# Kernel optimization log

Hardware: AMD Instinct MI355X
Metric: run time of the kernel (lower is better)

The kernel has to match this reference:

```python
import jax, jax.numpy as jnp
import numpy as np

NUM_NODES = 4000
SEQ_LEN = 96
LATENT_DIM = 32
GCN_LAYERS = 2
B = 4
NT = NUM_NODES + SEQ_LEN  # 4096


def setup_inputs() -> dict:
    key = jax.random.key(0)
    k_x, k_w = jax.random.split(key)
    X = jax.random.normal(k_x, (B, NT, LATENT_DIM), dtype=jnp.float32) * 0.1
    # per-layer weights for the graph conv (HeteroFASTGCN-style message passing)
    W = jax.random.normal(k_w, (GCN_LAYERS, LATENT_DIM, LATENT_DIM), dtype=jnp.float32) * (1.0 / np.sqrt(LATENT_DIM))
    return {"X": X, "W": W}


def reference(X, W):
    # STGraphConstructor: node_embs = concat(spatial, temporal) == X
    # adj = tanh(relu(X X^T) + I); dense equivalent of the per-batch nonzero
    # edge extraction (sparse edges carry exactly the nonzero adj entries,
    # so weighted scatter-aggregation == adj @ H).
    sim = jnp.einsum('bnf,bmf->bnm', X, X)          # (B, NT, NT)
    eye = jnp.eye(NT, dtype=X.dtype)
    adj = jnp.tanh(jax.nn.relu(sim) + eye)
    # graph conv: gcn_layers of weighted aggregation + linear + elu
    H = X
    for l in range(GCN_LAYERS):
        H = jax.nn.elu(jnp.einsum('bnm,bmf,fg->bng', adj, H, W[l]))
    # GraphEmbeeding is identity on H
    return H
```

## Files before the change

kernel.cpp:

```cpp
#include <hip/hip_runtime.h>

#define NTOT 4096
#define FD 32
#define BATCH 4

typedef __attribute__((ext_vector_type(8))) _Float16 half8;
typedef __attribute__((ext_vector_type(4))) _Float16 half4;
typedef __attribute__((ext_vector_type(2))) _Float16 half2v;
typedef __attribute__((ext_vector_type(4))) float f32x4;

__device__ __forceinline__ float tanh_pos(float t) {
    float u = __builtin_amdgcn_exp2f(t * 2.885390081777927f);
    float r = __builtin_amdgcn_rcpf(u + 1.0f);
    return __builtin_fmaf(-2.0f, r, 1.0f);
}

__device__ __forceinline__ float tanh_poly_f32(float t) {
    float t2 = t * t;
    float c = __builtin_fmaf(t2, 0.1333333333f, -0.3333333333f);
    return __builtin_fmaf(t * t2, c, t);
}

__device__ __forceinline__ float eluf(float x) {
    return x > 0.0f ? x : (__builtin_amdgcn_exp2f(x * 1.4426950408889634f) - 1.0f);
}

__device__ __forceinline__ half4 pack_relu_poly(f32x4 s) {
    half2v a = __builtin_bit_cast(half2v, __builtin_amdgcn_cvt_pkrtz(s[0], s[1]));
    half2v b = __builtin_bit_cast(half2v, __builtin_amdgcn_cvt_pkrtz(s[2], s[3]));
    const half2v zero = {(_Float16)0.0f, (_Float16)0.0f};
    const half2v mth = {(_Float16)(-0.33333334f), (_Float16)(-0.33333334f)};
    const half2v one = {(_Float16)1.0f, (_Float16)1.0f};
    a = __builtin_elementwise_max(a, zero);
    b = __builtin_elementwise_max(b, zero);
    half2v a2 = a * a, b2 = b * b;
    half2v ca = a2 * mth + one, cb = b2 * mth + one;
    a = a * ca;
    b = b * cb;
    return __builtin_shufflevector(a, b, 0, 1, 2, 3);
}

__global__ __launch_bounds__(256) void convert_x(const float* __restrict__ X,
                                                 _Float16* __restrict__ Kfrag,
                                                 _Float16* __restrict__ Vfrag) {
    __shared__ float lds[128 * 33];
    const int tid = threadIdx.x;
    const int blk = blockIdx.x;
    const int xcd = blk & 7;
    const int batch = xcd >> 1;
    const int chunk = ((xcd & 1) << 4) | (blk >> 3);
    const int nbase = chunk << 7;

    const float* Xp = X + ((size_t)batch * NTOT + nbase) * FD;
#pragma unroll
    for (int k = 0; k < 16; ++k) {
        int e = tid + k * 256;
        lds[(e >> 5) * 33 + (e & 31)] = Xp[e];
    }
    __syncthreads();

    {
        _Float16* kout = Kfrag + (size_t)batch * NTOT * FD + (size_t)(nbase >> 4) * 512;
        const int tl = tid >> 5;
        const int l0 = (tid & 31) * 2;
#pragma unroll
        for (int s = 0; s < 2; ++s) {
            int l = l0 + s;
            int row = tl * 16 + (l & 15);
            int cb = (l >> 4) * 8;
            half8 v;
#pragma unroll
            for (int j = 0; j < 8; ++j) v[j] = (_Float16)lds[row * 33 + cb + j];
            *(half8*)(kout + (tl * 64 + l) * 8) = v;
        }
    }
    {
        _Float16* vout = Vfrag + (size_t)batch * NTOT * FD + (size_t)(nbase >> 4) * 512;
        const int tl = tid >> 5;
        const int fh = (tid >> 4) & 1;
        const int lb = (tid & 15) * 4;
#pragma unroll
        for (int li = 0; li < 4; ++li) {
            int lane = lb + li;
            int l15 = lane & 15, lg = lane >> 4;
            half4 v;
#pragma unroll
            for (int j = 0; j < 4; ++j)
                v[j] = (_Float16)lds[(tl * 16 + lg * 4 + j) * 33 + fh * 16 + l15];
            *(half4*)(vout + ((tl * 2 + fh) * 64 + lane) * 4) = v;
        }
    }
}

template <int LAYER>
__global__ __launch_bounds__(512, 4) void gcn_layer_kernel(const _Float16* __restrict__ Kf,
                                                           const _Float16* __restrict__ Vf,
                                                           const float* __restrict__ Wg,
                                                           _Float16* __restrict__ outHt,
                                                           float* __restrict__ outF) {
    __shared__ float lds_part[8 * 32 * 32];

    const int tid = threadIdx.x;
    const int lane = tid & 63;
    const int wv = tid >> 6;
    const int blk = blockIdx.x;
    const int xcd = blk & 7;
    const int b = xcd >> 1;
    const int rowbase = ((((xcd & 1) << 6) + (blk >> 3))) << 5;
    const int l15 = lane & 15;
    const int lg = lane >> 4;

    const _Float16* KfB = Kf + (size_t)b * NTOT * FD;
    const _Float16* VfB = Vf + (size_t)b * NTOT * FD;

    const half8 q1 = *(const half8*)(KfB + (size_t)(rowbase >> 4) * 512 + lane * 8);
    const half8 q2 = *(const half8*)(KfB + (size_t)((rowbase >> 4) + 1) * 512 + lane * 8);

    const int col0 = wv << 9;
    const _Float16* kq = KfB + (size_t)(col0 >> 4) * 512 + lane * 8;
    const _Float16* vq = VfB + (size_t)(col0 >> 4) * 512 + lane * 4;

    f32x4 accA0 = {0.f, 0.f, 0.f, 0.f}, accA1 = {0.f, 0.f, 0.f, 0.f};
    f32x4 accB0 = {0.f, 0.f, 0.f, 0.f}, accB1 = {0.f, 0.f, 0.f, 0.f};
    const f32x4 zero = {0.f, 0.f, 0.f, 0.f};

    const int diag_it = (rowbase - col0) >> 5;

#pragma unroll
    for (int it = 0; it < 16; ++it) {
        half8 k0 = *(const half8*)(kq + it * 1024);
        half8 k1 = *(const half8*)(kq + it * 1024 + 512);
        half4 v00 = *(const half4*)(vq + it * 1024);
        half4 v01 = *(const half4*)(vq + it * 1024 + 256);
        half4 v10 = *(const half4*)(vq + it * 1024 + 512);
        half4 v11 = *(const half4*)(vq + it * 1024 + 768);

        f32x4 s00 = __builtin_amdgcn_mfma_f32_16x16x32_f16(k0, q1, zero, 0, 0, 0);
        f32x4 s01 = __builtin_amdgcn_mfma_f32_16x16x32_f16(k0, q2, zero, 0, 0, 0);
        f32x4 s10 = __builtin_amdgcn_mfma_f32_16x16x32_f16(k1, q1, zero, 0, 0, 0);
        f32x4 s11 = __builtin_amdgcn_mfma_f32_16x16x32_f16(k1, q2, zero, 0, 0, 0);

        half4 p00, p01, p10, p11;
        if (it == diag_it) {
            float t00[4], t01[4], t10[4], t11[4];
#pragma unroll
            for (int e = 0; e < 4; ++e) {
                t00[e] = fmaxf(s00[e], 0.0f);
                t01[e] = fmaxf(s01[e], 0.0f);
                t10[e] = fmaxf(s10[e], 0.0f);
                t11[e] = fmaxf(s11[e], 0.0f);
            }
#pragma unroll
            for (int e = 0; e < 4; ++e) {
                bool d = (lg * 4 + e == l15);
                t00[e] = d ? tanh_pos(t00[e] + 1.0f) : tanh_poly_f32(t00[e]);
                t11[e] = d ? tanh_pos(t11[e] + 1.0f) : tanh_poly_f32(t11[e]);
                t01[e] = tanh_poly_f32(t01[e]);
                t10[e] = tanh_poly_f32(t10[e]);
            }
            p00 = __builtin_shufflevector(
                __builtin_bit_cast(half2v, __builtin_amdgcn_cvt_pkrtz(t00[0], t00[1])),
                __builtin_bit_cast(half2v, __builtin_amdgcn_cvt_pkrtz(t00[2], t00[3])), 0, 1, 2, 3);
            p01 = __builtin_shufflevector(
                __builtin_bit_cast(half2v, __builtin_amdgcn_cvt_pkrtz(t01[0], t01[1])),
                __builtin_bit_cast(half2v, __builtin_amdgcn_cvt_pkrtz(t01[2], t01[3])), 0, 1, 2, 3);
            p10 = __builtin_shufflevector(
                __builtin_bit_cast(half2v, __builtin_amdgcn_cvt_pkrtz(t10[0], t10[1])),
                __builtin_bit_cast(half2v, __builtin_amdgcn_cvt_pkrtz(t10[2], t10[3])), 0, 1, 2, 3);
            p11 = __builtin_shufflevector(
                __builtin_bit_cast(half2v, __builtin_amdgcn_cvt_pkrtz(t11[0], t11[1])),
                __builtin_bit_cast(half2v, __builtin_amdgcn_cvt_pkrtz(t11[2], t11[3])), 0, 1, 2, 3);
        } else {
            p00 = pack_relu_poly(s00);
            p01 = pack_relu_poly(s01);
            p10 = pack_relu_poly(s10);
            p11 = pack_relu_poly(s11);
        }

        accA0 = __builtin_amdgcn_mfma_f32_16x16x16f16(v00, p00, accA0, 0, 0, 0);
        accA1 = __builtin_amdgcn_mfma_f32_16x16x16f16(v00, p01, accA1, 0, 0, 0);
        accB0 = __builtin_amdgcn_mfma_f32_16x16x16f16(v01, p00, accB0, 0, 0, 0);
        accB1 = __builtin_amdgcn_mfma_f32_16x16x16f16(v01, p01, accB1, 0, 0, 0);
        accA0 = __builtin_amdgcn_mfma_f32_16x16x16f16(v10, p10, accA0, 0, 0, 0);
        accA1 = __builtin_amdgcn_mfma_f32_16x16x16f16(v10, p11, accA1, 0, 0, 0);
        accB0 = __builtin_amdgcn_mfma_f32_16x16x16f16(v11, p10, accB0, 0, 0, 0);
        accB1 = __builtin_amdgcn_mfma_f32_16x16x16f16(v11, p11, accB1, 0, 0, 0);
    }

#pragma unroll
    for (int e = 0; e < 4; ++e) {
        int f0 = lg * 4 + e;
        lds_part[(wv * 32 + f0) * 32 + l15] = accA0[e];
        lds_part[(wv * 32 + f0) * 32 + 16 + l15] = accA1[e];
        lds_part[(wv * 32 + 16 + f0) * 32 + l15] = accB0[e];
        lds_part[(wv * 32 + 16 + f0) * 32 + 16 + l15] = accB1[e];
    }
    __syncthreads();

#pragma unroll
    for (int k = 0; k < 2; ++k) {
        int o = tid + k * 512;
        float ssum = 0.0f;
#pragma unroll
        for (int ww = 0; ww < 8; ++ww) ssum += lds_part[ww * 1024 + o];
        lds_part[o] = ssum;
    }
    __syncthreads();

    if (LAYER == 0) {
        const int jp = tid & 1;
        const int vlane = (tid >> 1) & 63;
        const int fh = (tid >> 7) & 1;
        const int tl = tid >> 8;
        const int vl15 = vlane & 15, vlg = vlane >> 4;
        const int g = fh * 16 + vl15;
        const int r0 = tl * 16 + vlg * 4 + jp * 2;
        float a0 = 0.0f, a1 = 0.0f;
#pragma unroll
        for (int f = 0; f < FD; ++f) {
            float w = Wg[f * FD + g];
            a0 = __builtin_fmaf(lds_part[f * 32 + r0], w, a0);
            a1 = __builtin_fmaf(lds_part[f * 32 + r0 + 1], w, a1);
        }
        a0 = eluf(a0);
        a1 = eluf(a1);
        unsigned pk = __builtin_bit_cast(unsigned, __builtin_amdgcn_cvt_pkrtz(a0, a1));
        _Float16* dst = outHt + (size_t)b * NTOT * FD +
                        ((size_t)(((rowbase >> 4) + tl) * 2 + fh) * 64 + vlane) * 4 + jp * 2;
        *(unsigned*)dst = pk;
    } else {
        const int g = tid & 31, r0 = tid >> 5;
        float a0 = 0.0f, a1 = 0.0f;
#pragma unroll
        for (int f = 0; f < FD; ++f) {
            float w = Wg[f * FD + g];
            a0 = __builtin_fmaf(lds_part[f * 32 + r0], w, a0);
            a1 = __builtin_fmaf(lds_part[f * 32 + r0 + 16], w, a1);
        }
        a0 = eluf(a0);
        a1 = eluf(a1);
        float* dst = outF + ((size_t)b * NTOT + rowbase) * FD + g;
        dst[(size_t)r0 * FD] = a0;
        dst[(size_t)(r0 + 16) * FD] = a1;
    }
}

extern "C" void kernel_launch(void* const* d_in, const int* in_sizes, int n_in,
                              void* d_out, int out_size, void* d_ws, size_t ws_size,
                              hipStream_t stream) {
    const float* X = (const float*)d_in[0];
    const float* W = (const float*)d_in[1];
    float* out = (float*)d_out;

    _Float16* Kfrag = (_Float16*)d_ws;
    _Float16* VfragX = Kfrag + (size_t)BATCH * NTOT * FD;
    _Float16* H1frag = VfragX + (size_t)BATCH * NTOT * FD;

    convert_x<<<128, 256, 0, stream>>>(X, Kfrag, VfragX);
    gcn_layer_kernel<0><<<512, 512, 0, stream>>>(Kfrag, VfragX, W, H1frag, nullptr);
    gcn_layer_kernel<1><<<512, 512, 0, stream>>>(Kfrag, H1frag, W + FD * FD, nullptr, out);
}
```

Before: 41.67 us.

## Process 64 rows per block with 16 waves and fp16 partial reduction

Each block now covers 64 query rows using 1024 threads (16 waves), and each wave handles 256 key columns across four query tiles. Every K/V fragment load now feeds four query tiles instead of two, which cuts global traffic per output and halves the grid to 256 blocks. Cross-wave partial sums are stored in LDS as fp16 to fit the larger reduction, at some precision cost. Fewer blocks on a large chip and more registers per thread may reduce occupancy.

```diff
diff --git a/kernel.cpp b/kernel.cpp
--- a/kernel.cpp
+++ b/kernel.cpp
@@ -40,6 +40,20 @@
     return __builtin_shufflevector(a, b, 0, 1, 2, 3);
 }
 
+__device__ __forceinline__ half4 diag_transform(f32x4 s, int l15, int lg) {
+    float t[4];
+#pragma unroll
+    for (int e = 0; e < 4; ++e) t[e] = fmaxf(s[e], 0.0f);
+#pragma unroll
+    for (int e = 0; e < 4; ++e) {
+        bool d = (lg * 4 + e == l15);
+        t[e] = d ? tanh_pos(t[e] + 1.0f) : tanh_poly_f32(t[e]);
+    }
+    return __builtin_shufflevector(
+        __builtin_bit_cast(half2v, __builtin_amdgcn_cvt_pkrtz(t[0], t[1])),
+        __builtin_bit_cast(half2v, __builtin_amdgcn_cvt_pkrtz(t[2], t[3])), 0, 1, 2, 3);
+}
+
 __global__ __launch_bounds__(256) void convert_x(const float* __restrict__ X,
                                                  _Float16* __restrict__ Kfrag,
                                                  _Float16* __restrict__ Vfrag) {
@@ -93,12 +107,12 @@
 }
 
 template <int LAYER>
-__global__ __launch_bounds__(512, 4) void gcn_layer_kernel(const _Float16* __restrict__ Kf,
-                                                           const _Float16* __restrict__ Vf,
-                                                           const float* __restrict__ Wg,
-                                                           _Float16* __restrict__ outHt,
-                                                           float* __restrict__ outF) {
-    __shared__ float lds_part[8 * 32 * 32];
+__global__ __launch_bounds__(1024, 4) void gcn_layer_kernel(const _Float16* __restrict__ Kf,
+                                                            const _Float16* __restrict__ Vf,
+                                                            const float* __restrict__ Wg,
+                                                            _Float16* __restrict__ outHt,
+                                                            float* __restrict__ outF) {
+    __shared__ _Float16 lds_part[16 * 64 * 32];
 
     const int tid = threadIdx.x;
     const int lane = tid & 63;
@@ -106,127 +120,119 @@
     const int blk = blockIdx.x;
     const int xcd = blk & 7;
     const int b = xcd >> 1;
-    const int rowbase = ((((xcd & 1) << 6) + (blk >> 3))) << 5;
+    const int rowidx = ((xcd & 1) << 5) | (blk >> 3);
+    const int rowbase = rowidx << 6;
     const int l15 = lane & 15;
     const int lg = lane >> 4;
 
     const _Float16* KfB = Kf + (size_t)b * NTOT * FD;
     const _Float16* VfB = Vf + (size_t)b * NTOT * FD;
 
-    const half8 q1 = *(const half8*)(KfB + (size_t)(rowbase >> 4) * 512 + lane * 8);
-    const half8 q2 = *(const half8*)(KfB + (size_t)((rowbase >> 4) + 1) * 512 + lane * 8);
-
-    const int col0 = wv << 9;
+    half8 q[4];
+#pragma unroll
+    for (int qt = 0; qt < 4; ++qt)
+        q[qt] = *(const half8*)(KfB + (size_t)((rowbase >> 4) + qt) * 512 + lane * 8);
+
+    const int col0 = wv << 8;
     const _Float16* kq = KfB + (size_t)(col0 >> 4) * 512 + lane * 8;
     const _Float16* vq = VfB + (size_t)(col0 >> 4) * 512 + lane * 4;
 
-    f32x4 accA0 = {0.f, 0.f, 0.f, 0.f}, accA1 = {0.f, 0.f, 0.f, 0.f};
-    f32x4 accB0 = {0.f, 0.f, 0.f, 0.f}, accB1 = {0.f, 0.f, 0.f, 0.f};
+    f32x4 accA[4], accB[4];
+#pragma unroll
+    for (int qt = 0; qt < 4; ++qt) {
+        accA[qt] = (f32x4){0.f, 0.f, 0.f, 0.f};
+        accB[qt] = (f32x4){0.f, 0.f, 0.f, 0.f};
+    }
     const f32x4 zero = {0.f, 0.f, 0.f, 0.f};
 
-    const int diag_it = (rowbase - col0) >> 5;
-
-#pragma unroll
-    for (int it = 0; it < 16; ++it) {
-        half8 k0 = *(const half8*)(kq + it * 1024);
-        half8 k1 = *(const half8*)(kq + it * 1024 + 512);
-        half4 v00 = *(const half4*)(vq + it * 1024);
-        half4 v01 = *(const half4*)(vq + it * 1024 + 256);
-        half4 v10 = *(const half4*)(vq + it * 1024 + 512);
-        half4 v11 = *(const half4*)(vq + it * 1024 + 768);
-
-        f32x4 s00 = __builtin_amdgcn_mfma_f32_16x16x32_f16(k0, q1, zero, 0, 0, 0);
-        f32x4 s01 = __builtin_amdgcn_mfma_f32_16x16x32_f16(k0, q2, zero, 0, 0, 0);
-        f32x4 s10 = __builtin_amdgcn_mfma_f32_16x16x32_f16(k1, q1, zero, 0, 0, 0);
-        f32x4 s11 = __builtin_amdgcn_mfma_f32_16x16x32_f16(k1, q2, zero, 0, 0, 0);
-
-        half4 p00, p01, p10, p11;
-        if (it == diag_it) {
-            float t00[4], t01[4], t10[4], t11[4];
-#pragma unroll
-            for (int e = 0; e < 4; ++e) {
-                t00[e] = fmaxf(s00[e], 0.0f);
-                t01[e] = fmaxf(s01[e], 0.0f);
-                t10[e] = fmaxf(s10[e], 0.0f);
-                t11[e] = fmaxf(s11[e], 0.0f);
-            }
-#pragma unroll
-            for (int e = 0; e < 4; ++e) {
-                bool d = (lg * 4 + e == l15);
-                t00[e] = d ? tanh_pos(t00[e] + 1.0f) : tanh_poly_f32(t00[e]);
-                t11[e] = d ? tanh_pos(t11[e] + 1.0f) : tanh_poly_f32(t11[e]);
-                t01[e] = tanh_poly_f32(t01[e]);
-                t10[e] = tanh_poly_f32(t10[e]);
-            }
-            p00 = __builtin_shufflevector(
-                __builtin_bit_cast(half2v, __builtin_amdgcn_cvt_pkrtz(t00[0], t00[1])),
-                __builtin_bit_cast(half2v, __builtin_amdgcn_cvt_pkrtz(t00[2], t00[3])), 0, 1, 2, 3);
-            p01 = __builtin_shufflevector(
-                __builtin_bit_cast(half2v, __builtin_amdgcn_cvt_pkrtz(t01[0], t01[1])),
-                __builtin_bit_cast(half2v, __builtin_amdgcn_cvt_pkrtz(t01[2], t01[3])), 0, 1, 2, 3);
-            p10 = __builtin_shufflevector(
-                __builtin_bit_cast(half2v, __builtin_amdgcn_cvt_pkrtz(t10[0], t10[1])),
-                __builtin_bit_cast(half2v, __builtin_amdgcn_cvt_pkrtz(t10[2], t10[3])), 0, 1, 2, 3);
-            p11 = __builtin_shufflevector(
-                __builtin_bit_cast(half2v, __builtin_amdgcn_cvt_pkrtz(t11[0], t11[1])),
-                __builtin_bit_cast(half2v, __builtin_amdgcn_cvt_pkrtz(t11[2], t11[3])), 0, 1, 2, 3);
-        } else {
-            p00 = pack_relu_poly(s00);
-            p01 = pack_relu_poly(s01);
-            p10 = pack_relu_poly(s10);
-            p11 = pack_relu_poly(s11);
-        }
-
-        accA0 = __builtin_amdgcn_mfma_f32_16x16x16f16(v00, p00, accA0, 0, 0, 0);
-        accA1 = __builtin_amdgcn_mfma_f32_16x16x16f16(v00, p01, accA1, 0, 0, 0);
-        accB0 = __builtin_amdgcn_mfma_f32_16x16x16f16(v01, p00, accB0, 0, 0, 0);
-        accB1 = __builtin_amdgcn_mfma_f32_16x16x16f16(v01, p01, accB1, 0, 0, 0);
-        accA0 = __builtin_amdgcn_mfma_f32_16x16x16f16(v10, p10, accA0, 0, 0, 0);
-        accA1 = __builtin_amdgcn_mfma_f32_16x16x16f16(v10, p11, accA1, 0, 0, 0);
-        accB0 = __builtin_amdgcn_mfma_f32_16x16x16f16(v11, p10, accB0, 0, 0, 0);
-        accB1 = __builtin_amdgcn_mfma_f32_16x16x16f16(v11, p11, accB1, 0, 0, 0);
-    }
-
-#pragma unroll
-    for (int e = 0; e < 4; ++e) {
-        int f0 = lg * 4 + e;
-        lds_part[(wv * 32 + f0) * 32 + l15] = accA0[e];
-        lds_part[(wv * 32 + f0) * 32 + 16 + l15] = accA1[e];
-        lds_part[(wv * 32 + 16 + f0) * 32 + l15] = accB0[e];
-        lds_part[(wv * 32 + 16 + f0) * 32 + 16 + l15] = accB1[e];
-    }
-    __syncthreads();
-
-#pragma unroll
-    for (int k = 0; k < 2; ++k) {
-        int o = tid + k * 512;
-        float ssum = 0.0f;
-#pragma unroll
-        for (int ww = 0; ww < 8; ++ww) ssum += lds_part[ww * 1024 + o];
-        lds_part[o] = ssum;
-    }
+    const int diagA = (rowbase - col0) >> 5;
+
+#pragma unroll
+    for (int it = 0; it < 8; ++it) {
+        const int base = it * 1024;
+        half8 k0 = *(const half8*)(kq + base);
+        half8 k1 = *(const half8*)(kq + base + 512);
+        half4 v00 = *(const half4*)(vq + base);
+        half4 v01 = *(const half4*)(vq + base + 256);
+        half4 v10 = *(const half4*)(vq + base + 512);
+        half4 v11 = *(const half4*)(vq + base + 768);
+
+        f32x4 s0[4], s1[4];
+#pragma unroll
+        for (int qt = 0; qt < 4; ++qt) {
+            s0[qt] = __builtin_amdgcn_mfma_f32_16x16x32_f16(k0, q[qt], zero, 0, 0, 0);
+            s1[qt] = __builtin_amdgcn_mfma_f32_16x16x32_f16(k1, q[qt], zero, 0, 0, 0);
+        }
+
+        half4 p0[4], p1[4];
+#pragma unroll
+        for (int qt = 0; qt < 4; ++qt) {
+            p0[qt] = pack_relu_poly(s0[qt]);
+            p1[qt] = pack_relu_poly(s1[qt]);
+        }
+        if (it == diagA) {
+            p0[0] = diag_transform(s0[0], l15, lg);
+            p1[1] = diag_transform(s1[1], l15, lg);
+        }
+        if (it == diagA + 1) {
+            p0[2] = diag_transform(s0[2], l15, lg);
+            p1[3] = diag_transform(s1[3], l15, lg);
+        }
+
+#pragma unroll
+        for (int qt = 0; qt < 4; ++qt) {
+            accA[qt] = __builtin_amdgcn_mfma_f32_16x16x16f16(v00, p0[qt], accA[qt], 0, 0, 0);
+            accB[qt] = __builtin_amdgcn_mfma_f32_16x16x16f16(v01, p0[qt], accB[qt], 0, 0, 0);
+            accA[qt] = __builtin_amdgcn_mfma_f32_16x16x16f16(v10, p1[qt], accA[qt], 0, 0, 0);
+            accB[qt] = __builtin_amdgcn_mfma_f32_16x16x16f16(v11, p1[qt], accB[qt], 0, 0, 0);
+        }
+    }
+
+#pragma unroll
+    for (int qt = 0; qt < 4; ++qt) {
+        half4 pa = __builtin_shufflevector(
+            __builtin_bit_cast(half2v, __builtin_amdgcn_cvt_pkrtz(accA[qt][0], accA[qt][1])),
+            __builtin_bit_cast(half2v, __builtin_amdgcn_cvt_pkrtz(accA[qt][2], accA[qt][3])), 0, 1, 2, 3);
+        half4 pb = __builtin_shufflevector(
+            __builtin_bit_cast(half2v, __builtin_amdgcn_cvt_pkrtz(accB[qt][0], accB[qt][1])),
+            __builtin_bit_cast(half2v, __builtin_amdgcn_cvt_pkrtz(accB[qt][2], accB[qt][3])), 0, 1, 2, 3);
+        int r = qt * 16 + l15;
+        *(half4*)(lds_part + (wv * 64 + r) * 32 + lg * 4) = pa;
+        *(half4*)(lds_part + (wv * 64 + r) * 32 + 16 + lg * 4) = pb;
+    }
+    __syncthreads();
+
+    float red0 = 0.0f, red1 = 0.0f;
+#pragma unroll
+    for (int ww = 0; ww < 16; ++ww) {
+        red0 += (float)lds_part[ww * 2048 + tid];
+        red1 += (float)lds_part[ww * 2048 + tid + 1024];
+    }
+    __syncthreads();
+    float* ldsf = (float*)lds_part;
+    ldsf[tid] = red0;
+    ldsf[tid + 1024] = red1;
     __syncthreads();
 
     if (LAYER == 0) {
         const int jp = tid & 1;
-        const int vlane = (tid >> 1) & 63;
+        const int lane_v = (tid >> 1) & 63;
         const int fh = (tid >> 7) & 1;
         const int tl = tid >> 8;
-        const int vl15 = vlane & 15, vlg = vlane >> 4;
-        const int g = fh * 16 + vl15;
-        const int r0 = tl * 16 + vlg * 4 + jp * 2;
+        const int g = fh * 16 + (lane_v & 15);
+        const int r0 = tl * 16 + ((lane_v >> 4) << 2) + jp * 2;
         float a0 = 0.0f, a1 = 0.0f;
 #pragma unroll
         for (int f = 0; f < FD; ++f) {
             float w = Wg[f * FD + g];
-            a0 = __builtin_fmaf(lds_part[f * 32 + r0], w, a0);
-            a1 = __builtin_fmaf(lds_part[f * 32 + r0 + 1], w, a1);
+            a0 = __builtin_fmaf(ldsf[r0 * FD + f], w, a0);
+            a1 = __builtin_fmaf(ldsf[(r0 + 1) * FD + f], w, a1);
         }
         a0 = eluf(a0);
         a1 = eluf(a1);
         unsigned pk = __builtin_bit_cast(unsigned, __builtin_amdgcn_cvt_pkrtz(a0, a1));
         _Float16* dst = outHt + (size_t)b * NTOT * FD +
-                        ((size_t)(((rowbase >> 4) + tl) * 2 + fh) * 64 + vlane) * 4 + jp * 2;
+                        ((size_t)(((rowbase >> 4) + tl) * 2 + fh) * 64 + lane_v) * 4 + jp * 2;
         *(unsigned*)dst = pk;
     } else {
         const int g = tid & 31, r0 = tid >> 5;
@@ -234,14 +240,14 @@
 #pragma unroll
         for (int f = 0; f < FD; ++f) {
             float w = Wg[f * FD + g];
-            a0 = __builtin_fmaf(lds_part[f * 32 + r0], w, a0);
-            a1 = __builtin_fmaf(lds_part[f * 32 + r0 + 16], w, a1);
+            a0 = __builtin_fmaf(ldsf[r0 * FD + f], w, a0);
+            a1 = __builtin_fmaf(ldsf[(r0 + 32) * FD + f], w, a1);
         }
         a0 = eluf(a0);
         a1 = eluf(a1);
         float* dst = outF + ((size_t)b * NTOT + rowbase) * FD + g;
         dst[(size_t)r0 * FD] = a0;
-        dst[(size_t)(r0 + 16) * FD] = a1;
+        dst[(size_t)(r0 + 32) * FD] = a1;
     }
 }
 
@@ -257,6 +263,6 @@
     _Float16* H1frag = VfragX + (size_t)BATCH * NTOT * FD;
 
     convert_x<<<128, 256, 0, stream>>>(X, Kfrag, VfragX);
-    gcn_layer_kernel<0><<<512, 512, 0, stream>>>(Kfrag, VfragX, W, H1frag, nullptr);
-    gcn_layer_kernel<1><<<512, 512, 0, stream>>>(Kfrag, H1frag, W + FD * FD, nullptr, out);
-}
+    gcn_layer_kernel<0><<<256, 1024, 0, stream>>>(Kfrag, VfragX, W, H1frag, nullptr);
+    gcn_layer_kernel<1><<<256, 1024, 0, stream>>>(Kfrag, H1frag, W + FD * FD, nullptr, out);
+}
```

After: 37.34 us. -10.4%, faster.
